# Kernel tuning notes

Measured on AMD Instinct MI355X. Metric: run time of the kernel, lower is better.

Reference implementation:

```python
import jax, jax.numpy as jnp
import numpy as np

N = 10000
E = 160000
UNITS = 64
NUM_RBF = 32
CUTOFF = 1.0


def _xavier(k, shape):
    fan_out, fan_in = shape
    lim = float(np.sqrt(6.0 / (fan_in + fan_out)))
    return jax.random.uniform(k, shape, minval=-lim, maxval=lim, dtype=jnp.float32)


def setup_inputs() -> dict:
    key = jax.random.key(0)
    ks = jax.random.split(key, 16)
    inp = {
        "edge_index": jax.random.randint(ks[0], (2, E), 0, N),
        "edge_weight": jax.random.uniform(ks[1], (E,), dtype=jnp.float32),
        "edge_attr": jax.random.normal(ks[2], (E, NUM_RBF), dtype=jnp.float32),
        "X": jax.random.normal(ks[3], (N, UNITS, 3, 3), dtype=jnp.float32),
        # scalar MLP: num_rbf -> units -> 2*units -> 3*units
        "Ws0": _xavier(ks[4], (UNITS, NUM_RBF)), "bs0": jnp.zeros((UNITS,), jnp.float32),
        "Ws1": _xavier(ks[5], (2 * UNITS, UNITS)), "bs1": jnp.zeros((2 * UNITS,), jnp.float32),
        "Ws2": _xavier(ks[6], (3 * UNITS, 2 * UNITS)), "bs2": jnp.zeros((3 * UNITS,), jnp.float32),
    }
    for i in range(6):
        inp[f"Wt{i}"] = _xavier(ks[7 + i], (UNITS, UNITS))
    return inp


def cosine_cutoff(r, cutoff):
    return jnp.where(r < cutoff, 0.5 * (jnp.cos(jnp.pi * r / cutoff) + 1.0), 0.0)


def tensor_norm(X):
    # X: [N, units, 3, 3] -> [N, units]
    return jnp.sum(X * X, axis=(-2, -1))


def decompose_tensor(X):
    eye = jnp.eye(3, dtype=X.dtype)
    trace = jnp.trace(X, axis1=-2, axis2=-1)  # [N, units]
    I = (trace / 3.0)[..., None, None] * eye
    A = 0.5 * (X - jnp.swapaxes(X, -2, -1))
    S = 0.5 * (X + jnp.swapaxes(X, -2, -1)) - I
    return I, A, S


def channel_linear(T, W):
    # linear over the channel dim: [N, c, 3, 3] x [d, c] -> [N, d, 3, 3]
    return jnp.einsum('ncij,dc->ndij', T, W)


def reference(edge_index, edge_weight, edge_attr, X,
              Ws0, bs0, Ws1, bs1, Ws2, bs2,
              Wt0, Wt1, Wt2, Wt3, Wt4, Wt5):
    act = jax.nn.silu
    C = cosine_cutoff(edge_weight, CUTOFF)  # [E]
    h = act(edge_attr @ Ws0.T + bs0)
    h = act(h @ Ws1.T + bs1)
    h = act(h @ Ws2.T + bs2)  # [E, 3*units]
    ea = (h * C[:, None]).reshape(h.shape[0], UNITS, 3)  # [E, units, 3]

    X = X / (tensor_norm(X) + 1.0)[..., None, None]
    I, A, S = decompose_tensor(X)
    I = channel_linear(I, Wt0)
    A = channel_linear(A, Wt1)
    S = channel_linear(S, Wt2)
    Y = I + A + S

    src, dst = edge_index[0], edge_index[1]
    n = X.shape[0]
    # message = per-edge radial scaling of gathered node tensors; aggregate at src
    Im = jax.ops.segment_sum(ea[..., 0, None, None] * I[dst], src, num_segments=n)
    Am = jax.ops.segment_sum(ea[..., 1, None, None] * A[dst], src, num_segments=n)
    Sm = jax.ops.segment_sum(ea[..., 2, None, None] * S[dst], src, num_segments=n)
    msg = Im + Am + Sm

    # O(3): symmetrized product of batched 3x3 matmuls
    AB = jnp.matmul(msg, Y) + jnp.matmul(Y, msg)
    I2, A2, S2 = decompose_tensor(AB)
    normp1 = (tensor_norm(I2 + A2 + S2) + 1.0)[..., None, None]
    I2 = channel_linear(I2 / normp1, Wt3)
    A2 = channel_linear(A2 / normp1, Wt4)
    S2 = channel_linear(S2 / normp1, Wt5)
    dX = I2 + A2 + S2
    return X + dX + jnp.matmul(dX, dX)
```

## Files before the change

kernel.cpp:

```cpp
#include <hip/hip_runtime.h>
#include <math.h>

#define NN 10000
#define EE 160000

#define OFF_WTT 0
#define OFF_PK  24576
#define OFF_B2P 41984
#define OFF_IASH 42176
#define OFF_EAH 3242176
#define OFF_INT 18602176

typedef __attribute__((ext_vector_type(8))) _Float16 h16x8;
typedef __attribute__((ext_vector_type(2))) __fp16 fp16x2_raw;
typedef __attribute__((ext_vector_type(4))) float f32x4;

__device__ __forceinline__ float silu_f(float x) {
    return x * __builtin_amdgcn_rcpf(1.0f + __expf(-x));
}
__device__ __forceinline__ unsigned int pkh(float a, float b) {
    union { fp16x2_raw h; unsigned int u; } cv;
    cv.h = __builtin_amdgcn_cvt_pkrtz(a, b);
    return cv.u;
}
__device__ __forceinline__ unsigned short f2h(float f) {
    union { _Float16 h; unsigned short u; } cv; cv.h = (_Float16)f; return cv.u;
}
__device__ __forceinline__ float h2f(unsigned short s) {
    union { unsigned short u; _Float16 h; } cv; cv.u = s; return (float)cv.h;
}
__device__ __forceinline__ float h2f_lo(unsigned int u) { return h2f((unsigned short)(u & 0xffffu)); }
__device__ __forceinline__ float h2f_hi(unsigned int u) { return h2f((unsigned short)(u >> 16)); }

__global__ void k_prep(const float* __restrict__ Wt0, const float* __restrict__ Wt1,
                       const float* __restrict__ Wt2, const float* __restrict__ Wt3,
                       const float* __restrict__ Wt4, const float* __restrict__ Wt5,
                       const float* __restrict__ Ws0, const float* __restrict__ Ws1,
                       const float* __restrict__ Ws2, const float* __restrict__ bs2,
                       const int* __restrict__ ei,
                       float* __restrict__ WtT, unsigned short* __restrict__ PK,
                       float* __restrict__ bs2p, int* __restrict__ counts) {
    int idx = blockIdx.x * 256 + threadIdx.x;
    if (idx < 24576) {
        int k = idx >> 12, r = idx & 4095;
        int c = r >> 6, d = r & 63;
        const float* W = (k == 0) ? Wt0 : (k == 1) ? Wt1 : (k == 2) ? Wt2
                       : (k == 3) ? Wt3 : (k == 4) ? Wt4 : Wt5;
        WtT[idx] = W[d * 64 + c];
    } else if (idx < 26624) {
        int q = idx - 24576;
        int ot = q >> 9, r = q & 511, lane = r >> 3, j = r & 7;
        int k = ((lane >> 4) * 8) + j, o = ot * 16 + (lane & 15);
        PK[q] = f2h(Ws0[o * 32 + k]);
    } else if (idx < 34816) {
        int q = idx - 24576;
        int i = q - 2048, ch = i >> 9, r = i & 511, lane = r >> 3, j = r & 7;
        int ot = ch >> 1, ks = ch & 1;
        int k = ks * 32 + (lane >> 4) * 8 + j, o = ot * 16 + (lane & 15);
        PK[q] = f2h(Ws1[o * 64 + k]);
    } else if (idx < 59392) {
        int q = idx - 24576;
        int i = q - 10240, ch = i >> 9, r = i & 511, lane = r >> 3, j = r & 7;
        int ot = ch >> 2, ks = ch & 3;
        int k = ks * 32 + (lane >> 4) * 8 + j;
        int op = ot * 16 + (lane & 15);
        int o = (op & 63) * 3 + (op >> 6);
        PK[q] = f2h(Ws2[o * 128 + k]);
    } else if (idx < 59584) {
        int op = idx - 59392;
        bs2p[op] = bs2[(op & 63) * 3 + (op >> 6)];
    } else if (idx < 59584 + EE) {
        int e = idx - 59584;
        atomicAdd(&counts[ei[e]], 1);
    }
}

__global__ __launch_bounds__(256) void k_scan(const int* __restrict__ counts,
                                              int* __restrict__ offsets) {
    __shared__ int sums[256];
    int t = threadIdx.x;
    int base = t * 40;
    int s = 0;
    if (base < NN) {
        const int4* p = (const int4*)(counts + base);
#pragma unroll
        for (int q = 0; q < 10; ++q) { int4 a = p[q]; s += a.x + a.y + a.z + a.w; }
    }
    sums[t] = s;
    __syncthreads();
    for (int off = 1; off < 256; off <<= 1) {
        int tmp = (t >= off) ? sums[t - off] : 0;
        __syncthreads();
        sums[t] += tmp;
        __syncthreads();
    }
    int run = sums[t] - s;
    if (base < NN) {
        const int4* p = (const int4*)(counts + base);
#pragma unroll
        for (int q = 0; q < 10; ++q) {
            int4 a = p[q];
            offsets[base + 4 * q + 0] = run; run += a.x;
            offsets[base + 4 * q + 1] = run; run += a.y;
            offsets[base + 4 * q + 2] = run; run += a.z;
            offsets[base + 4 * q + 3] = run; run += a.w;
        }
    }
    if (t == 255) offsets[NN] = run;
}

__global__ void k_fill(const int* __restrict__ ei, const int* __restrict__ offsets,
                       int* __restrict__ cursor, int* __restrict__ bucket,
                       int* __restrict__ dstp) {
    int e = blockIdx.x * 256 + threadIdx.x;
    if (e < EE) {
        int s = ei[e];
        int pos = offsets[s] + atomicAdd(&cursor[s], 1);
        bucket[pos] = e;
        dstp[pos] = ei[EE + e];
    }
}

__global__ __launch_bounds__(256) void k_nodeprep(const float* __restrict__ X,
                                                  const float* __restrict__ WtT,
                                                  unsigned int* __restrict__ IASu) {
    int t = threadIdx.x, w = t >> 6, c = t & 63;
    int n = blockIdx.x * 4 + w;
    __shared__ float XS[4][576];
    __shared__ float L[4][64][12];
    float* xs = XS[w];
#pragma unroll
    for (int i = 0; i < 9; i++) xs[c + 64 * i] = X[(size_t)n * 576 + c + 64 * i];
    __builtin_amdgcn_wave_barrier();
    float x[9];
#pragma unroll
    for (int j = 0; j < 9; j++) x[j] = xs[c * 9 + j];
    float nrm = 0.f;
#pragma unroll
    for (int j = 0; j < 9; j++) nrm += x[j] * x[j];
    float inv = __builtin_amdgcn_rcpf(nrm + 1.0f);
#pragma unroll
    for (int j = 0; j < 9; j++) x[j] *= inv;
    float tr3 = (x[0] + x[4] + x[8]) * (1.0f / 3.0f);
    L[w][c][0] = tr3;
    L[w][c][1] = 0.5f * (x[1] - x[3]);
    L[w][c][2] = 0.5f * (x[2] - x[6]);
    L[w][c][3] = 0.5f * (x[5] - x[7]);
    L[w][c][4] = x[0] - tr3;
    L[w][c][5] = x[4] - tr3;
    L[w][c][6] = 0.5f * (x[1] + x[3]);
    L[w][c][7] = 0.5f * (x[2] + x[6]);
    L[w][c][8] = 0.5f * (x[5] + x[7]);
    __builtin_amdgcn_wave_barrier();
    int d = c;
    const float* W0 = WtT;
    const float* W1 = WtT + 4096;
    const float* W2 = WtT + 8192;
    float aI = 0, aA0 = 0, aA1 = 0, aA2 = 0, aS0 = 0, aS1 = 0, aS2 = 0, aS3 = 0, aS4 = 0;
    for (int cc = 0; cc < 64; ++cc) {
        float w0 = W0[cc * 64 + d], w1 = W1[cc * 64 + d], w2 = W2[cc * 64 + d];
        float4 L0 = *(const float4*)&L[w][cc][0];
        float4 L1 = *(const float4*)&L[w][cc][4];
        float L8 = L[w][cc][8];
        aI  += w0 * L0.x;
        aA0 += w1 * L0.y; aA1 += w1 * L0.z; aA2 += w1 * L0.w;
        aS0 += w2 * L1.x; aS1 += w2 * L1.y; aS2 += w2 * L1.z;
        aS3 += w2 * L1.w; aS4 += w2 * L8;
    }
    unsigned int* op = IASu + (size_t)n * 320 + d;
    op[0]   = pkh(aI, aA0);
    op[64]  = pkh(aA1, aA2);
    op[128] = pkh(aS0, aS1);
    op[192] = pkh(aS2, aS3);
    op[256] = pkh(aS4, 0.0f);
}

__global__ __launch_bounds__(256) void k_mlp(const float* __restrict__ attr,
                                             const float* __restrict__ ew,
                                             const int* __restrict__ bucket,
                                             const unsigned short* __restrict__ PK,
                                             const float* __restrict__ bs0,
                                             const float* __restrict__ bs1,
                                             const float* __restrict__ bs2p,
                                             unsigned short* __restrict__ eah) {
    __shared__ unsigned short H[4][16][152];
    int t = threadIdx.x;
    int l = t & 63, w = t >> 6, lr = l & 15, lg = l >> 4;
    int pos = blockIdx.x * 64 + w * 16 + lr;
    int eid = bucket[pos];
    const float* ap = attr + (size_t)eid * 32 + lg * 8;
    float4 av0 = *(const float4*)ap;
    float4 av1 = *(const float4*)(ap + 4);
    union { h16x8 h; unsigned int u[4]; } B1;
    B1.u[0] = pkh(av0.x, av0.y); B1.u[1] = pkh(av0.z, av0.w);
    B1.u[2] = pkh(av1.x, av1.y); B1.u[3] = pkh(av1.z, av1.w);
    float rw = ew[eid];
    float C = (rw < 1.0f) ? 0.5f * (cosf(3.14159265358979f * rw) + 1.0f) : 0.0f;

    const h16x8* P1 = (const h16x8*)PK;
    const h16x8* P2 = (const h16x8*)(PK + 2048);
    const h16x8* P3 = (const h16x8*)(PK + 10240);

#pragma unroll
    for (int ot = 0; ot < 4; ++ot) {
        float4 bb = *(const float4*)&bs0[ot * 16 + lg * 4];
        f32x4 acc = {bb.x, bb.y, bb.z, bb.w};
        acc = __builtin_amdgcn_mfma_f32_16x16x32_f16(P1[ot * 64 + l], B1.h, acc, 0, 0, 0);
        unsigned int u01 = pkh(silu_f(acc[0]), silu_f(acc[1]));
        unsigned int u23 = pkh(silu_f(acc[2]), silu_f(acc[3]));
        *(uint2*)&H[w][lr][ot * 16 + lg * 4] = make_uint2(u01, u23);
    }
    __builtin_amdgcn_wave_barrier();

    h16x8 B2a = *(const h16x8*)&H[w][lr][lg * 8];
    h16x8 B2b = *(const h16x8*)&H[w][lr][32 + lg * 8];
    __builtin_amdgcn_wave_barrier();
#pragma unroll
    for (int ot = 0; ot < 8; ++ot) {
        float4 bb = *(const float4*)&bs1[ot * 16 + lg * 4];
        f32x4 acc = {bb.x, bb.y, bb.z, bb.w};
        acc = __builtin_amdgcn_mfma_f32_16x16x32_f16(P2[(ot * 2 + 0) * 64 + l], B2a, acc, 0, 0, 0);
        acc = __builtin_amdgcn_mfma_f32_16x16x32_f16(P2[(ot * 2 + 1) * 64 + l], B2b, acc, 0, 0, 0);
        unsigned int u01 = pkh(silu_f(acc[0]), silu_f(acc[1]));
        unsigned int u23 = pkh(silu_f(acc[2]), silu_f(acc[3]));
        *(uint2*)&H[w][lr][ot * 16 + lg * 4] = make_uint2(u01, u23);
    }
    __builtin_amdgcn_wave_barrier();

    h16x8 B3[4];
#pragma unroll
    for (int ks = 0; ks < 4; ++ks)
        B3[ks] = *(const h16x8*)&H[w][lr][ks * 32 + lg * 8];
    size_t ebase = (size_t)pos * 192;
#pragma unroll
    for (int ot = 0; ot < 12; ++ot) {
        float4 bb = *(const float4*)&bs2p[ot * 16 + lg * 4];
        f32x4 acc = {bb.x, bb.y, bb.z, bb.w};
#pragma unroll
        for (int ks = 0; ks < 4; ++ks)
            acc = __builtin_amdgcn_mfma_f32_16x16x32_f16(P3[(ot * 4 + ks) * 64 + l], B3[ks], acc, 0, 0, 0);
        unsigned int u01 = pkh(silu_f(acc[0]) * C, silu_f(acc[1]) * C);
        unsigned int u23 = pkh(silu_f(acc[2]) * C, silu_f(acc[3]) * C);
        *(uint2*)&eah[ebase + ot * 16 + lg * 4] = make_uint2(u01, u23);
    }
}

__global__ __launch_bounds__(256) void k_aggout(const int* __restrict__ offsets,
                                                const int* __restrict__ dstp,
                                                const unsigned short* __restrict__ eah,
                                                const unsigned int* __restrict__ IASu,
                                                const float* __restrict__ X,
                                                const float* __restrict__ WtT,
                                                float* __restrict__ out) {
    int t = threadIdx.x, w = t >> 6, c = t & 63;
    int n = blockIdx.x * 4 + w;
    __shared__ float XS[4][576];
    __shared__ float LO[4][768];
    float* xs = XS[w];
    float* lo = LO[w];
#pragma unroll
    for (int i = 0; i < 9; i++) xs[c + 64 * i] = X[(size_t)n * 576 + c + 64 * i];

    int beg = offsets[n], end = offsets[n + 1];
    float m0 = 0, m1 = 0, m2 = 0, m3 = 0, m4 = 0, m5 = 0, m6 = 0, m7 = 0, m8 = 0;
    int i = beg;
    for (; i + 2 <= end; i += 2) {
        int d0 = dstp[i], d1 = dstp[i + 1];
        const unsigned short* ep0 = eah + (size_t)i * 192;
        const unsigned short* ep1 = ep0 + 192;
        float a00 = h2f(ep0[c]), a01 = h2f(ep0[64 + c]), a02 = h2f(ep0[128 + c]);
        float a10 = h2f(ep1[c]), a11 = h2f(ep1[64 + c]), a12 = h2f(ep1[128 + c]);
        const unsigned int* p0 = IASu + (size_t)d0 * 320 + c;
        const unsigned int* p1 = IASu + (size_t)d1 * 320 + c;
        unsigned int u00 = p0[0], u01 = p0[64], u02 = p0[128], u03 = p0[192], u04 = p0[256];
        unsigned int u10 = p1[0], u11 = p1[64], u12 = p1[128], u13 = p1[192], u14 = p1[256];
        m0 += a00 * h2f_lo(u00) + a10 * h2f_lo(u10);
        m1 += a01 * h2f_hi(u00) + a11 * h2f_hi(u10);
        m2 += a01 * h2f_lo(u01) + a11 * h2f_lo(u11);
        m3 += a01 * h2f_hi(u01) + a11 * h2f_hi(u11);
        m4 += a02 * h2f_lo(u02) + a12 * h2f_lo(u12);
        m5 += a02 * h2f_hi(u02) + a12 * h2f_hi(u12);
        m6 += a02 * h2f_lo(u03) + a12 * h2f_lo(u13);
        m7 += a02 * h2f_hi(u03) + a12 * h2f_hi(u13);
        m8 += a02 * h2f_lo(u04) + a12 * h2f_lo(u14);
    }
    if (i < end) {
        int d0 = dstp[i];
        const unsigned short* ep0 = eah + (size_t)i * 192;
        float a00 = h2f(ep0[c]), a01 = h2f(ep0[64 + c]), a02 = h2f(ep0[128 + c]);
        const unsigned int* p0 = IASu + (size_t)d0 * 320 + c;
        unsigned int u00 = p0[0], u01 = p0[64], u02 = p0[128], u03 = p0[192], u04 = p0[256];
        m0 += a00 * h2f_lo(u00); m1 += a01 * h2f_hi(u00);
        m2 += a01 * h2f_lo(u01); m3 += a01 * h2f_hi(u01);
        m4 += a02 * h2f_lo(u02); m5 += a02 * h2f_hi(u02);
        m6 += a02 * h2f_lo(u03); m7 += a02 * h2f_hi(u03);
        m8 += a02 * h2f_lo(u04);
    }
    const unsigned int* yp = IASu + (size_t)n * 320 + c;
    unsigned int y0 = yp[0], y1 = yp[64], y2 = yp[128], y3 = yp[192], y4 = yp[256];
    float yI = h2f_lo(y0), yA0 = h2f_hi(y0), yA1 = h2f_lo(y1), yA2 = h2f_hi(y1);
    float yS0 = h2f_lo(y2), yS1 = h2f_hi(y2), yS2 = h2f_lo(y3), yS3 = h2f_hi(y3);
    float yS4 = h2f_lo(y4);

    float M[3][3] = {
        { m0 + m4,   m1 + m6,  m2 + m7 },
        { -m1 + m6,  m0 + m5,  m3 + m8 },
        { -m2 + m7, -m3 + m8,  m0 - m4 - m5 } };
    float Y[3][3] = {
        { yI + yS0,   yA0 + yS2,  yA1 + yS3 },
        { -yA0 + yS2, yI + yS1,   yA2 + yS4 },
        { -yA1 + yS3, -yA2 + yS4, yI - yS0 - yS1 } };
    float AB[3][3];
#pragma unroll
    for (int ii = 0; ii < 3; ii++)
#pragma unroll
        for (int j = 0; j < 3; j++) {
            float s = 0.f;
#pragma unroll
            for (int k = 0; k < 3; k++) s += M[ii][k] * Y[k][j] + Y[ii][k] * M[k][j];
            AB[ii][j] = s;
        }
    float tr3 = (AB[0][0] + AB[1][1] + AB[2][2]) * (1.0f / 3.0f);
    float fro = 0.f;
#pragma unroll
    for (int ii = 0; ii < 3; ii++)
#pragma unroll
        for (int j = 0; j < 3; j++) fro += AB[ii][j] * AB[ii][j];
    float inv = __builtin_amdgcn_rcpf(fro + 1.0f);
    float (*L12)[12] = (float (*)[12])lo;
    L12[c][0] = tr3 * inv;
    L12[c][1] = 0.5f * (AB[0][1] - AB[1][0]) * inv;
    L12[c][2] = 0.5f * (AB[0][2] - AB[2][0]) * inv;
    L12[c][3] = 0.5f * (AB[1][2] - AB[2][1]) * inv;
    L12[c][4] = (AB[0][0] - tr3) * inv;
    L12[c][5] = (AB[1][1] - tr3) * inv;
    L12[c][6] = 0.5f * (AB[0][1] + AB[1][0]) * inv;
    L12[c][7] = 0.5f * (AB[0][2] + AB[2][0]) * inv;
    L12[c][8] = 0.5f * (AB[1][2] + AB[2][1]) * inv;
    __builtin_amdgcn_wave_barrier();
    int d = c;
    const float* W3 = WtT + 3 * 4096;
    const float* W4 = WtT + 4 * 4096;
    const float* W5 = WtT + 5 * 4096;
    float aI = 0, aA0 = 0, aA1 = 0, aA2 = 0, aS0 = 0, aS1 = 0, aS2 = 0, aS3 = 0, aS4 = 0;
    for (int cc = 0; cc < 64; ++cc) {
        float w3 = W3[cc * 64 + d], w4 = W4[cc * 64 + d], w5 = W5[cc * 64 + d];
        float4 L0 = *(const float4*)&L12[cc][0];
        float4 L1 = *(const float4*)&L12[cc][4];
        float L8 = L12[cc][8];
        aI  += w3 * L0.x;
        aA0 += w4 * L0.y; aA1 += w4 * L0.z; aA2 += w4 * L0.w;
        aS0 += w5 * L1.x; aS1 += w5 * L1.y; aS2 += w5 * L1.z;
        aS3 += w5 * L1.w; aS4 += w5 * L8;
    }
    float dX[3][3] = {
        { aI + aS0,   aA0 + aS2,  aA1 + aS3 },
        { -aA0 + aS2, aI + aS1,   aA2 + aS4 },
        { -aA1 + aS3, -aA2 + aS4, aI - aS0 - aS1 } };
    float D2[3][3];
#pragma unroll
    for (int ii = 0; ii < 3; ii++)
#pragma unroll
        for (int j = 0; j < 3; j++) {
            float s = 0.f;
#pragma unroll
            for (int k = 0; k < 3; k++) s += dX[ii][k] * dX[k][j];
            D2[ii][j] = s;
        }
    float x[9];
    __builtin_amdgcn_wave_barrier();
#pragma unroll
    for (int j = 0; j < 9; j++) x[j] = xs[d * 9 + j];
    float nrm = 0.f;
#pragma unroll
    for (int j = 0; j < 9; j++) nrm += x[j] * x[j];
    float xinv = __builtin_amdgcn_rcpf(nrm + 1.0f);
    __builtin_amdgcn_wave_barrier();
#pragma unroll
    for (int ii = 0; ii < 3; ii++)
#pragma unroll
        for (int j = 0; j < 3; j++)
            lo[d * 9 + ii * 3 + j] = x[ii * 3 + j] * xinv + dX[ii][j] + D2[ii][j];
    __builtin_amdgcn_wave_barrier();
#pragma unroll
    for (int ii = 0; ii < 9; ii++) out[(size_t)n * 576 + c + 64 * ii] = lo[c + 64 * ii];
}

extern "C" void kernel_launch(void* const* d_in, const int* in_sizes, int n_in,
                              void* d_out, int out_size, void* d_ws, size_t ws_size,
                              hipStream_t stream) {
    (void)in_sizes; (void)n_in; (void)out_size; (void)ws_size;
    const int* ei = (const int*)d_in[0];
    const float* ew = (const float*)d_in[1];
    const float* attr = (const float*)d_in[2];
    const float* X = (const float*)d_in[3];
    const float* Ws0 = (const float*)d_in[4];
    const float* bs0 = (const float*)d_in[5];
    const float* Ws1 = (const float*)d_in[6];
    const float* bs1 = (const float*)d_in[7];
    const float* Ws2 = (const float*)d_in[8];
    const float* bs2 = (const float*)d_in[9];
    const float* Wt0 = (const float*)d_in[10];
    const float* Wt1 = (const float*)d_in[11];
    const float* Wt2 = (const float*)d_in[12];
    const float* Wt3 = (const float*)d_in[13];
    const float* Wt4 = (const float*)d_in[14];
    const float* Wt5 = (const float*)d_in[15];
    float* ws = (float*)d_ws;
    int* ibase = (int*)(ws + OFF_INT);
    int* counts = ibase;
    int* cursor = ibase + NN;
    int* offsets = ibase + 2 * NN;
    int* bucket = ibase + 3 * NN + 1;
    int* dstp = bucket + EE;
    unsigned short* PK = (unsigned short*)(ws + OFF_PK);
    unsigned int* IASu = (unsigned int*)(ws + OFF_IASH);
    unsigned short* eah = (unsigned short*)(ws + OFF_EAH);

    (void)hipMemsetAsync(counts, 0, 2 * NN * sizeof(int), stream);
    k_prep<<<(59584 + EE + 255) / 256, 256, 0, stream>>>(
        Wt0, Wt1, Wt2, Wt3, Wt4, Wt5, Ws0, Ws1, Ws2, bs2, ei,
        ws, PK, ws + OFF_B2P, counts);
    k_scan<<<1, 256, 0, stream>>>(counts, offsets);
    k_fill<<<(EE + 255) / 256, 256, 0, stream>>>(ei, offsets, cursor, bucket, dstp);
    k_nodeprep<<<NN / 4, 256, 0, stream>>>(X, ws, IASu);
    k_mlp<<<EE / 64, 256, 0, stream>>>(attr, ew, bucket, PK, bs0, bs1, ws + OFF_B2P, eah);
    k_aggout<<<NN / 4, 256, 0, stream>>>(offsets, dstp, eah, IASu, X, ws, (float*)d_out);
}
```

Measured before the change: 162.8 us.

## Batch four edge tiles per MLP wave, read weights untransposed, widen gather unroll

```diff
diff --git a/kernel.cpp b/kernel.cpp
--- a/kernel.cpp
+++ b/kernel.cpp
@@ -4,12 +4,11 @@
 #define NN 10000
 #define EE 160000
 
-#define OFF_WTT 0
-#define OFF_PK  24576
-#define OFF_B2P 41984
-#define OFF_IASH 42176
-#define OFF_EAH 3242176
-#define OFF_INT 18602176
+#define OFF_PK   0
+#define OFF_B2P  17408
+#define OFF_IASH 17600
+#define OFF_EAH  3217600
+#define OFF_INT  18577600
 
 typedef __attribute__((ext_vector_type(8))) _Float16 h16x8;
 typedef __attribute__((ext_vector_type(2))) __fp16 fp16x2_raw;
@@ -32,45 +31,36 @@
 __device__ __forceinline__ float h2f_lo(unsigned int u) { return h2f((unsigned short)(u & 0xffffu)); }
 __device__ __forceinline__ float h2f_hi(unsigned int u) { return h2f((unsigned short)(u >> 16)); }
 
-__global__ void k_prep(const float* __restrict__ Wt0, const float* __restrict__ Wt1,
-                       const float* __restrict__ Wt2, const float* __restrict__ Wt3,
-                       const float* __restrict__ Wt4, const float* __restrict__ Wt5,
-                       const float* __restrict__ Ws0, const float* __restrict__ Ws1,
+__global__ void k_prep(const float* __restrict__ Ws0, const float* __restrict__ Ws1,
                        const float* __restrict__ Ws2, const float* __restrict__ bs2,
                        const int* __restrict__ ei,
-                       float* __restrict__ WtT, unsigned short* __restrict__ PK,
+                       unsigned short* __restrict__ PK,
                        float* __restrict__ bs2p, int* __restrict__ counts) {
     int idx = blockIdx.x * 256 + threadIdx.x;
-    if (idx < 24576) {
-        int k = idx >> 12, r = idx & 4095;
-        int c = r >> 6, d = r & 63;
-        const float* W = (k == 0) ? Wt0 : (k == 1) ? Wt1 : (k == 2) ? Wt2
-                       : (k == 3) ? Wt3 : (k == 4) ? Wt4 : Wt5;
-        WtT[idx] = W[d * 64 + c];
-    } else if (idx < 26624) {
-        int q = idx - 24576;
+    if (idx < 2048) {
+        int q = idx;
         int ot = q >> 9, r = q & 511, lane = r >> 3, j = r & 7;
         int k = ((lane >> 4) * 8) + j, o = ot * 16 + (lane & 15);
         PK[q] = f2h(Ws0[o * 32 + k]);
-    } else if (idx < 34816) {
-        int q = idx - 24576;
+    } else if (idx < 10240) {
+        int q = idx;
         int i = q - 2048, ch = i >> 9, r = i & 511, lane = r >> 3, j = r & 7;
         int ot = ch >> 1, ks = ch & 1;
         int k = ks * 32 + (lane >> 4) * 8 + j, o = ot * 16 + (lane & 15);
         PK[q] = f2h(Ws1[o * 64 + k]);
-    } else if (idx < 59392) {
-        int q = idx - 24576;
+    } else if (idx < 34816) {
+        int q = idx;
         int i = q - 10240, ch = i >> 9, r = i & 511, lane = r >> 3, j = r & 7;
         int ot = ch >> 2, ks = ch & 3;
         int k = ks * 32 + (lane >> 4) * 8 + j;
         int op = ot * 16 + (lane & 15);
         int o = (op & 63) * 3 + (op >> 6);
         PK[q] = f2h(Ws2[o * 128 + k]);
-    } else if (idx < 59584) {
-        int op = idx - 59392;
+    } else if (idx < 35008) {
+        int op = idx - 34816;
         bs2p[op] = bs2[(op & 63) * 3 + (op >> 6)];
-    } else if (idx < 59584 + EE) {
-        int e = idx - 59584;
+    } else if (idx < 35008 + EE) {
+        int e = idx - 35008;
         atomicAdd(&counts[ei[e]], 1);
     }
 }
@@ -121,8 +111,21 @@
     }
 }
 
+#define CLSTEP(W0c, W1c, W2c, cc)                                             \
+    {                                                                          \
+        float4 L0 = *(const float4*)&L12[cc][0];                               \
+        float4 L1 = *(const float4*)&L12[cc][4];                               \
+        float L8 = L12[cc][8];                                                 \
+        aI  += (W0c) * L0.x;                                                   \
+        aA0 += (W1c) * L0.y; aA1 += (W1c) * L0.z; aA2 += (W1c) * L0.w;         \
+        aS0 += (W2c) * L1.x; aS1 += (W2c) * L1.y; aS2 += (W2c) * L1.z;         \
+        aS3 += (W2c) * L1.w; aS4 += (W2c) * L8;                                \
+    }
+
 __global__ __launch_bounds__(256) void k_nodeprep(const float* __restrict__ X,
-                                                  const float* __restrict__ WtT,
+                                                  const float* __restrict__ Wt0,
+                                                  const float* __restrict__ Wt1,
+                                                  const float* __restrict__ Wt2,
                                                   unsigned int* __restrict__ IASu) {
     int t = threadIdx.x, w = t >> 6, c = t & 63;
     int n = blockIdx.x * 4 + w;
@@ -153,19 +156,20 @@
     L[w][c][8] = 0.5f * (x[5] + x[7]);
     __builtin_amdgcn_wave_barrier();
     int d = c;
-    const float* W0 = WtT;
-    const float* W1 = WtT + 4096;
-    const float* W2 = WtT + 8192;
+    float (*L12)[12] = L[w];
+    const float* w0p = Wt0 + d * 64;
+    const float* w1p = Wt1 + d * 64;
+    const float* w2p = Wt2 + d * 64;
     float aI = 0, aA0 = 0, aA1 = 0, aA2 = 0, aS0 = 0, aS1 = 0, aS2 = 0, aS3 = 0, aS4 = 0;
-    for (int cc = 0; cc < 64; ++cc) {
-        float w0 = W0[cc * 64 + d], w1 = W1[cc * 64 + d], w2 = W2[cc * 64 + d];
-        float4 L0 = *(const float4*)&L[w][cc][0];
-        float4 L1 = *(const float4*)&L[w][cc][4];
-        float L8 = L[w][cc][8];
-        aI  += w0 * L0.x;
-        aA0 += w1 * L0.y; aA1 += w1 * L0.z; aA2 += w1 * L0.w;
-        aS0 += w2 * L1.x; aS1 += w2 * L1.y; aS2 += w2 * L1.z;
-        aS3 += w2 * L1.w; aS4 += w2 * L8;
+#pragma unroll
+    for (int cc4 = 0; cc4 < 16; ++cc4) {
+        float4 w0q = *(const float4*)&w0p[cc4 * 4];
+        float4 w1q = *(const float4*)&w1p[cc4 * 4];
+        float4 w2q = *(const float4*)&w2p[cc4 * 4];
+        CLSTEP(w0q.x, w1q.x, w2q.x, cc4 * 4 + 0);
+        CLSTEP(w0q.y, w1q.y, w2q.y, cc4 * 4 + 1);
+        CLSTEP(w0q.z, w1q.z, w2q.z, cc4 * 4 + 2);
+        CLSTEP(w0q.w, w1q.w, w2q.w, cc4 * 4 + 3);
     }
     unsigned int* op = IASu + (size_t)n * 320 + d;
     op[0]   = pkh(aI, aA0);
@@ -175,73 +179,100 @@
     op[256] = pkh(aS4, 0.0f);
 }
 
-__global__ __launch_bounds__(256) void k_mlp(const float* __restrict__ attr,
-                                             const float* __restrict__ ew,
-                                             const int* __restrict__ bucket,
-                                             const unsigned short* __restrict__ PK,
-                                             const float* __restrict__ bs0,
-                                             const float* __restrict__ bs1,
-                                             const float* __restrict__ bs2p,
-                                             unsigned short* __restrict__ eah) {
-    __shared__ unsigned short H[4][16][152];
+__global__ __launch_bounds__(256, 2) void k_mlp(const float* __restrict__ attr,
+                                                const float* __restrict__ ew,
+                                                const int* __restrict__ bucket,
+                                                const unsigned short* __restrict__ PK,
+                                                const float* __restrict__ bs0,
+                                                const float* __restrict__ bs1,
+                                                const float* __restrict__ bs2p,
+                                                unsigned short* __restrict__ eah) {
+    __shared__ unsigned short H[4][4][16][136];
     int t = threadIdx.x;
     int l = t & 63, w = t >> 6, lr = l & 15, lg = l >> 4;
-    int pos = blockIdx.x * 64 + w * 16 + lr;
-    int eid = bucket[pos];
-    const float* ap = attr + (size_t)eid * 32 + lg * 8;
-    float4 av0 = *(const float4*)ap;
-    float4 av1 = *(const float4*)(ap + 4);
-    union { h16x8 h; unsigned int u[4]; } B1;
-    B1.u[0] = pkh(av0.x, av0.y); B1.u[1] = pkh(av0.z, av0.w);
-    B1.u[2] = pkh(av1.x, av1.y); B1.u[3] = pkh(av1.z, av1.w);
-    float rw = ew[eid];
-    float C = (rw < 1.0f) ? 0.5f * (cosf(3.14159265358979f * rw) + 1.0f) : 0.0f;
-
+    int base = blockIdx.x * 256 + w * 64;
     const h16x8* P1 = (const h16x8*)PK;
     const h16x8* P2 = (const h16x8*)(PK + 2048);
     const h16x8* P3 = (const h16x8*)(PK + 10240);
 
+    union { h16x8 h; unsigned int u[4]; } B1[4];
+    float C[4];
+#pragma unroll
+    for (int tt = 0; tt < 4; ++tt) {
+        int eid = bucket[base + tt * 16 + lr];
+        const float* ap = attr + (size_t)eid * 32 + lg * 8;
+        float4 a0 = *(const float4*)ap;
+        float4 a1 = *(const float4*)(ap + 4);
+        B1[tt].u[0] = pkh(a0.x, a0.y); B1[tt].u[1] = pkh(a0.z, a0.w);
+        B1[tt].u[2] = pkh(a1.x, a1.y); B1[tt].u[3] = pkh(a1.z, a1.w);
+        float rw = ew[eid];
+        C[tt] = (rw < 1.0f) ? 0.5f * (cosf(3.14159265358979f * rw) + 1.0f) : 0.0f;
+    }
+
 #pragma unroll
     for (int ot = 0; ot < 4; ++ot) {
+        h16x8 wf = P1[ot * 64 + l];
         float4 bb = *(const float4*)&bs0[ot * 16 + lg * 4];
-        f32x4 acc = {bb.x, bb.y, bb.z, bb.w};
-        acc = __builtin_amdgcn_mfma_f32_16x16x32_f16(P1[ot * 64 + l], B1.h, acc, 0, 0, 0);
-        unsigned int u01 = pkh(silu_f(acc[0]), silu_f(acc[1]));
-        unsigned int u23 = pkh(silu_f(acc[2]), silu_f(acc[3]));
-        *(uint2*)&H[w][lr][ot * 16 + lg * 4] = make_uint2(u01, u23);
-    }
-    __builtin_amdgcn_wave_barrier();
-
-    h16x8 B2a = *(const h16x8*)&H[w][lr][lg * 8];
-    h16x8 B2b = *(const h16x8*)&H[w][lr][32 + lg * 8];
+#pragma unroll
+        for (int tt = 0; tt < 4; ++tt) {
+            f32x4 acc = {bb.x, bb.y, bb.z, bb.w};
+            acc = __builtin_amdgcn_mfma_f32_16x16x32_f16(wf, B1[tt].h, acc, 0, 0, 0);
+            unsigned int u01 = pkh(silu_f(acc[0]), silu_f(acc[1]));
+            unsigned int u23 = pkh(silu_f(acc[2]), silu_f(acc[3]));
+            *(uint2*)&H[w][tt][lr][ot * 16 + lg * 4] = make_uint2(u01, u23);
+        }
+    }
+    __builtin_amdgcn_wave_barrier();
+
+    h16x8 B2a[4], B2b[4];
+#pragma unroll
+    for (int tt = 0; tt < 4; ++tt) {
+        B2a[tt] = *(const h16x8*)&H[w][tt][lr][lg * 8];
+        B2b[tt] = *(const h16x8*)&H[w][tt][lr][32 + lg * 8];
+    }
     __builtin_amdgcn_wave_barrier();
 #pragma unroll
     for (int ot = 0; ot < 8; ++ot) {
+        h16x8 wf0 = P2[(ot * 2 + 0) * 64 + l];
+        h16x8 wf1 = P2[(ot * 2 + 1) * 64 + l];
         float4 bb = *(const float4*)&bs1[ot * 16 + lg * 4];
-        f32x4 acc = {bb.x, bb.y, bb.z, bb.w};
-        acc = __builtin_amdgcn_mfma_f32_16x16x32_f16(P2[(ot * 2 + 0) * 64 + l], B2a, acc, 0, 0, 0);
-        acc = __builtin_amdgcn_mfma_f32_16x16x32_f16(P2[(ot * 2 + 1) * 64 + l], B2b, acc, 0, 0, 0);
-        unsigned int u01 = pkh(silu_f(acc[0]), silu_f(acc[1]));
-        unsigned int u23 = pkh(silu_f(acc[2]), silu_f(acc[3]));
-        *(uint2*)&H[w][lr][ot * 16 + lg * 4] = make_uint2(u01, u23);
-    }
-    __builtin_amdgcn_wave_barrier();
-
-    h16x8 B3[4];
+#pragma unroll
+        for (int tt = 0; tt < 4; ++tt) {
+            f32x4 acc = {bb.x, bb.y, bb.z, bb.w};
+            acc = __builtin_amdgcn_mfma_f32_16x16x32_f16(wf0, B2a[tt], acc, 0, 0, 0);
+            acc = __builtin_amdgcn_mfma_f32_16x16x32_f16(wf1, B2b[tt], acc, 0, 0, 0);
+            unsigned int u01 = pkh(silu_f(acc[0]), silu_f(acc[1]));
+            unsigned int u23 = pkh(silu_f(acc[2]), silu_f(acc[3]));
+            *(uint2*)&H[w][tt][lr][ot * 16 + lg * 4] = make_uint2(u01, u23);
+        }
+    }
+    __builtin_amdgcn_wave_barrier();
+
+    h16x8 B3[4][4];
 #pragma unroll
     for (int ks = 0; ks < 4; ++ks)
-        B3[ks] = *(const h16x8*)&H[w][lr][ks * 32 + lg * 8];
-    size_t ebase = (size_t)pos * 192;
+#pragma unroll
+        for (int tt = 0; tt < 4; ++tt)
+            B3[ks][tt] = *(const h16x8*)&H[w][tt][lr][ks * 32 + lg * 8];
 #pragma unroll
     for (int ot = 0; ot < 12; ++ot) {
+        h16x8 wf0 = P3[(ot * 4 + 0) * 64 + l];
+        h16x8 wf1 = P3[(ot * 4 + 1) * 64 + l];
+        h16x8 wf2 = P3[(ot * 4 + 2) * 64 + l];
+        h16x8 wf3 = P3[(ot * 4 + 3) * 64 + l];
         float4 bb = *(const float4*)&bs2p[ot * 16 + lg * 4];
-        f32x4 acc = {bb.x, bb.y, bb.z, bb.w};
-#pragma unroll
-        for (int ks = 0; ks < 4; ++ks)
-            acc = __builtin_amdgcn_mfma_f32_16x16x32_f16(P3[(ot * 4 + ks) * 64 + l], B3[ks], acc, 0, 0, 0);
-        unsigned int u01 = pkh(silu_f(acc[0]) * C, silu_f(acc[1]) * C);
-        unsigned int u23 = pkh(silu_f(acc[2]) * C, silu_f(acc[3]) * C);
-        *(uint2*)&eah[ebase + ot * 16 + lg * 4] = make_uint2(u01, u23);
+#pragma unroll
+        for (int tt = 0; tt < 4; ++tt) {
+            f32x4 acc = {bb.x, bb.y, bb.z, bb.w};
+            acc = __builtin_amdgcn_mfma_f32_16x16x32_f16(wf0, B3[0][tt], acc, 0, 0, 0);
+            acc = __builtin_amdgcn_mfma_f32_16x16x32_f16(wf1, B3[1][tt], acc, 0, 0, 0);
+            acc = __builtin_amdgcn_mfma_f32_16x16x32_f16(wf2, B3[2][tt], acc, 0, 0, 0);
+            acc = __builtin_amdgcn_mfma_f32_16x16x32_f16(wf3, B3[3][tt], acc, 0, 0, 0);
+            unsigned int u01 = pkh(silu_f(acc[0]) * C[tt], silu_f(acc[1]) * C[tt]);
+            unsigned int u23 = pkh(silu_f(acc[2]) * C[tt], silu_f(acc[3]) * C[tt]);
+            *(uint2*)&eah[(size_t)(base + tt * 16 + lr) * 192 + ot * 16 + lg * 4]
+                = make_uint2(u01, u23);
+        }
     }
 }
 
@@ -250,7 +281,9 @@
                                                 const unsigned short* __restrict__ eah,
                                                 const unsigned int* __restrict__ IASu,
                                                 const float* __restrict__ X,
-                                                const float* __restrict__ WtT,
+                                                const float* __restrict__ Wt3,
+                                                const float* __restrict__ Wt4,
+                                                const float* __restrict__ Wt5,
                                                 float* __restrict__ out) {
     int t = threadIdx.x, w = t >> 6, c = t & 63;
     int n = blockIdx.x * 4 + w;
@@ -264,37 +297,35 @@
     int beg = offsets[n], end = offsets[n + 1];
     float m0 = 0, m1 = 0, m2 = 0, m3 = 0, m4 = 0, m5 = 0, m6 = 0, m7 = 0, m8 = 0;
     int i = beg;
-    for (; i + 2 <= end; i += 2) {
-        int d0 = dstp[i], d1 = dstp[i + 1];
-        const unsigned short* ep0 = eah + (size_t)i * 192;
-        const unsigned short* ep1 = ep0 + 192;
-        float a00 = h2f(ep0[c]), a01 = h2f(ep0[64 + c]), a02 = h2f(ep0[128 + c]);
-        float a10 = h2f(ep1[c]), a11 = h2f(ep1[64 + c]), a12 = h2f(ep1[128 + c]);
-        const unsigned int* p0 = IASu + (size_t)d0 * 320 + c;
-        const unsigned int* p1 = IASu + (size_t)d1 * 320 + c;
-        unsigned int u00 = p0[0], u01 = p0[64], u02 = p0[128], u03 = p0[192], u04 = p0[256];
-        unsigned int u10 = p1[0], u11 = p1[64], u12 = p1[128], u13 = p1[192], u14 = p1[256];
-        m0 += a00 * h2f_lo(u00) + a10 * h2f_lo(u10);
-        m1 += a01 * h2f_hi(u00) + a11 * h2f_hi(u10);
-        m2 += a01 * h2f_lo(u01) + a11 * h2f_lo(u11);
-        m3 += a01 * h2f_hi(u01) + a11 * h2f_hi(u11);
-        m4 += a02 * h2f_lo(u02) + a12 * h2f_lo(u12);
-        m5 += a02 * h2f_hi(u02) + a12 * h2f_hi(u12);
-        m6 += a02 * h2f_lo(u03) + a12 * h2f_lo(u13);
-        m7 += a02 * h2f_hi(u03) + a12 * h2f_hi(u13);
-        m8 += a02 * h2f_lo(u04) + a12 * h2f_lo(u14);
-    }
-    if (i < end) {
-        int d0 = dstp[i];
-        const unsigned short* ep0 = eah + (size_t)i * 192;
-        float a00 = h2f(ep0[c]), a01 = h2f(ep0[64 + c]), a02 = h2f(ep0[128 + c]);
-        const unsigned int* p0 = IASu + (size_t)d0 * 320 + c;
-        unsigned int u00 = p0[0], u01 = p0[64], u02 = p0[128], u03 = p0[192], u04 = p0[256];
-        m0 += a00 * h2f_lo(u00); m1 += a01 * h2f_hi(u00);
-        m2 += a01 * h2f_lo(u01); m3 += a01 * h2f_hi(u01);
-        m4 += a02 * h2f_lo(u02); m5 += a02 * h2f_hi(u02);
-        m6 += a02 * h2f_lo(u03); m7 += a02 * h2f_hi(u03);
-        m8 += a02 * h2f_lo(u04);
+    for (; i + 4 <= end; i += 4) {
+        float a[4][3];
+        unsigned int u[4][5];
+#pragma unroll
+        for (int q = 0; q < 4; ++q) {
+            const unsigned short* ep = eah + (size_t)(i + q) * 192;
+            a[q][0] = h2f(ep[c]); a[q][1] = h2f(ep[64 + c]); a[q][2] = h2f(ep[128 + c]);
+            const unsigned int* p = IASu + (size_t)dstp[i + q] * 320 + c;
+            u[q][0] = p[0]; u[q][1] = p[64]; u[q][2] = p[128]; u[q][3] = p[192]; u[q][4] = p[256];
+        }
+#pragma unroll
+        for (int q = 0; q < 4; ++q) {
+            m0 += a[q][0] * h2f_lo(u[q][0]); m1 += a[q][1] * h2f_hi(u[q][0]);
+            m2 += a[q][1] * h2f_lo(u[q][1]); m3 += a[q][1] * h2f_hi(u[q][1]);
+            m4 += a[q][2] * h2f_lo(u[q][2]); m5 += a[q][2] * h2f_hi(u[q][2]);
+            m6 += a[q][2] * h2f_lo(u[q][3]); m7 += a[q][2] * h2f_hi(u[q][3]);
+            m8 += a[q][2] * h2f_lo(u[q][4]);
+        }
+    }
+    for (; i < end; ++i) {
+        const unsigned short* ep = eah + (size_t)i * 192;
+        float a0 = h2f(ep[c]), a1 = h2f(ep[64 + c]), a2 = h2f(ep[128 + c]);
+        const unsigned int* p = IASu + (size_t)dstp[i] * 320 + c;
+        unsigned int u0 = p[0], u1 = p[64], u2 = p[128], u3 = p[192], u4 = p[256];
+        m0 += a0 * h2f_lo(u0); m1 += a1 * h2f_hi(u0);
+        m2 += a1 * h2f_lo(u1); m3 += a1 * h2f_hi(u1);
+        m4 += a2 * h2f_lo(u2); m5 += a2 * h2f_hi(u2);
+        m6 += a2 * h2f_lo(u3); m7 += a2 * h2f_hi(u3);
+        m8 += a2 * h2f_lo(u4);
     }
     const unsigned int* yp = IASu + (size_t)n * 320 + c;
     unsigned int y0 = yp[0], y1 = yp[64], y2 = yp[128], y3 = yp[192], y4 = yp[256];
@@ -339,19 +370,19 @@
     L12[c][8] = 0.5f * (AB[1][2] + AB[2][1]) * inv;
     __builtin_amdgcn_wave_barrier();
     int d = c;
-    const float* W3 = WtT + 3 * 4096;
-    const float* W4 = WtT + 4 * 4096;
-    const float* W5 = WtT + 5 * 4096;
+    const float* w3p = Wt3 + d * 64;
+    const float* w4p = Wt4 + d * 64;
+    const float* w5p = Wt5 + d * 64;
     float aI = 0, aA0 = 0, aA1 = 0, aA2 = 0, aS0 = 0, aS1 = 0, aS2 = 0, aS3 = 0, aS4 = 0;
-    for (int cc = 0; cc < 64; ++cc) {
-        float w3 = W3[cc * 64 + d], w4 = W4[cc * 64 + d], w5 = W5[cc * 64 + d];
-        float4 L0 = *(const float4*)&L12[cc][0];
-        float4 L1 = *(const float4*)&L12[cc][4];
-        float L8 = L12[cc][8];
-        aI  += w3 * L0.x;
-        aA0 += w4 * L0.y; aA1 += w4 * L0.z; aA2 += w4 * L0.w;
-        aS0 += w5 * L1.x; aS1 += w5 * L1.y; aS2 += w5 * L1.z;
-        aS3 += w5 * L1.w; aS4 += w5 * L8;
+#pragma unroll
+    for (int cc4 = 0; cc4 < 16; ++cc4) {
+        float4 w3q = *(const float4*)&w3p[cc4 * 4];
+        float4 w4q = *(const float4*)&w4p[cc4 * 4];
+        float4 w5q = *(const float4*)&w5p[cc4 * 4];
+        CLSTEP(w3q.x, w4q.x, w5q.x, cc4 * 4 + 0);
+        CLSTEP(w3q.y, w4q.y, w5q.y, cc4 * 4 + 1);
+        CLSTEP(w3q.z, w4q.z, w5q.z, cc4 * 4 + 2);
+        CLSTEP(w3q.w, w4q.w, w5q.w, cc4 * 4 + 3);
     }
     float dX[3][3] = {
         { aI + aS0,   aA0 + aS2,  aA1 + aS3 },
@@ -418,12 +449,12 @@
     unsigned short* eah = (unsigned short*)(ws + OFF_EAH);
 
     (void)hipMemsetAsync(counts, 0, 2 * NN * sizeof(int), stream);
-    k_prep<<<(59584 + EE + 255) / 256, 256, 0, stream>>>(
-        Wt0, Wt1, Wt2, Wt3, Wt4, Wt5, Ws0, Ws1, Ws2, bs2, ei,
-        ws, PK, ws + OFF_B2P, counts);
+    k_prep<<<(35008 + EE + 255) / 256, 256, 0, stream>>>(
+        Ws0, Ws1, Ws2, bs2, ei, PK, ws + OFF_B2P, counts);
     k_scan<<<1, 256, 0, stream>>>(counts, offsets);
     k_fill<<<(EE + 255) / 256, 256, 0, stream>>>(ei, offsets, cursor, bucket, dstp);
-    k_nodeprep<<<NN / 4, 256, 0, stream>>>(X, ws, IASu);
-    k_mlp<<<EE / 64, 256, 0, stream>>>(attr, ew, bucket, PK, bs0, bs1, ws + OFF_B2P, eah);
-    k_aggout<<<NN / 4, 256, 0, stream>>>(offsets, dstp, eah, IASu, X, ws, (float*)d_out);
-}
+    k_nodeprep<<<NN / 4, 256, 0, stream>>>(X, Wt0, Wt1, Wt2, IASu);
+    k_mlp<<<EE / 256, 256, 0, stream>>>(attr, ew, bucket, PK, bs0, bs1, ws + OFF_B2P, eah);
+    k_aggout<<<NN / 4, 256, 0, stream>>>(offsets, dstp, eah, IASu, X, Wt3, Wt4, Wt5,
+                                         (float*)d_out);
+}
```

Result: slower. 247.4 us (+52.0%).
